# Performance work log

Measured on AMD Instinct MI355X. Metric: run time of the kernel, lower is better.

Reference implementation:

```python
import jax, jax.numpy as jnp
import numpy as np

B, C, H, W = 64, 128, 32, 32
GROUPS = 32
EPS = 1e-6
SCALE = 0.044194173824159216  # 1/sqrt(512), as hardcoded in the torch module


def setup_inputs() -> dict:
    key = jax.random.key(0)
    ks = jax.random.split(key, 12)
    s = 1.0 / np.sqrt(C)
    return {
        "x": jax.random.normal(ks[0], (B, C, H, W), dtype=jnp.float32),
        "gn_w": jax.random.normal(ks[1], (C,), dtype=jnp.float32) * 0.02 + 1.0,
        "gn_b": jax.random.normal(ks[2], (C,), dtype=jnp.float32) * 0.02,
        "wq": jax.random.uniform(ks[3], (C, C), jnp.float32, -s, s),
        "bq": jax.random.uniform(ks[4], (C,), jnp.float32, -s, s),
        "wk": jax.random.uniform(ks[5], (C, C), jnp.float32, -s, s),
        "bk": jax.random.uniform(ks[6], (C,), jnp.float32, -s, s),
        "wv": jax.random.uniform(ks[7], (C, C), jnp.float32, -s, s),
        "bv": jax.random.uniform(ks[8], (C,), jnp.float32, -s, s),
        "wo": jax.random.uniform(ks[9], (C, C), jnp.float32, -s, s),
        "bo": jax.random.uniform(ks[10], (C,), jnp.float32, -s, s),
    }


def reference(x, gn_w, gn_b, wq, bq, wk, bk, wv, bv, wo, bo):
    b = x.shape[0]
    res = x
    # GroupNorm(32 groups, 128 channels): normalize over (channels_per_group, H, W)
    xg = x.reshape(b, GROUPS, C // GROUPS, H * W)
    mean = xg.mean(axis=(2, 3), keepdims=True)
    var = xg.var(axis=(2, 3), keepdims=True)
    xn = (xg - mean) * jax.lax.rsqrt(var + EPS)
    xn = xn.reshape(b, C, H, W) * gn_w[:, None, None] + gn_b[:, None, None]
    # flatten spatial -> sequence: [b, S=1024, C=128]
    t = xn.reshape(b, C, H * W).transpose(0, 2, 1)
    q = t @ wq.T + bq
    k = t @ wk.T + bk
    v = t @ wv.T + bv
    att = jnp.einsum('bsc,btc->bst', q, k) * SCALE  # [b, S, S]
    att = jax.nn.softmax(att, axis=-1)
    o = jnp.einsum('bst,btc->bsc', att, v)
    o = o @ wo.T + bo
    out = o.transpose(0, 2, 1).reshape(b, C, H, W) + res
    return out
```

## Files before the change

kernel.cpp:

```cpp
#include <hip/hip_runtime.h>
#include <hip/hip_bf16.h>

#define BATCH 64
#define CCH 128
#define SEQ 1024
#define NG 32
#define EPSV 1e-6f
#define SCALEV 0.044194173824159216f
#define QPRE (0.044194173824159216f * 1.4426950408889634f)

typedef short v8s __attribute__((ext_vector_type(8)));
typedef short v4s __attribute__((ext_vector_type(4)));
typedef float v4f __attribute__((ext_vector_type(4)));
typedef int   v4i __attribute__((ext_vector_type(4)));
typedef unsigned short us;

__device__ __forceinline__ us f2bf(float f) {
    __hip_bfloat16 h = __float2bfloat16(f);
    return *reinterpret_cast<us*>(&h);
}

__device__ __forceinline__ int cvtpk(float lo, float hi) {
    int r;
    asm("v_cvt_pk_bf16_f32 %0, %1, %2" : "=v"(r) : "v"(lo), "v"(hi));
    return r;
}

#if __has_builtin(__builtin_amdgcn_exp2f)
#define EXP2F(x) __builtin_amdgcn_exp2f(x)
#else
#define EXP2F(x) exp2f(x)
#endif

#define MFMA16(a, b, c) __builtin_amdgcn_mfma_f32_16x16x32_bf16(a, b, c, 0, 0, 0)

__device__ __forceinline__ void gld_lds16(const us* g, us* l) {
    __builtin_amdgcn_global_load_lds(
        (const __attribute__((address_space(1))) void*)g,
        (__attribute__((address_space(3))) void*)l, 16, 0, 0);
}

__global__ void prep_gn(const float* __restrict__ wq, const float* __restrict__ wk,
                        const float* __restrict__ wv, const float* __restrict__ wo,
                        us* wbf, const float* __restrict__ x,
                        float* meanr, float* rstdr) {
    int tid = threadIdx.x;
    if (blockIdx.x < 256) {
        int i = blockIdx.x * 256 + tid;
        const float* srcs[4] = {wq, wk, wv, wo};
        wbf[i] = f2bf(srcs[i >> 14][i & 16383]);
        return;
    }
    int bg = blockIdx.x - 256;
    const float4* p = (const float4*)(x + (size_t)bg * (4 * SEQ));
    float s1 = 0.f, s2 = 0.f;
    #pragma unroll
    for (int i = 0; i < 4; i++) {
        float4 v = p[i * 256 + tid];
        s1 += v.x + v.y + v.z + v.w;
        s2 += v.x * v.x + v.y * v.y + v.z * v.z + v.w * v.w;
    }
    #pragma unroll
    for (int off = 32; off; off >>= 1) {
        s1 += __shfl_down(s1, off);
        s2 += __shfl_down(s2, off);
    }
    __shared__ float a1[4], a2[4];
    int w = tid >> 6, l = tid & 63;
    if (l == 0) { a1[w] = s1; a2[w] = s2; }
    __syncthreads();
    if (tid == 0) {
        float t1 = a1[0] + a1[1] + a1[2] + a1[3];
        float t2 = a2[0] + a2[1] + a2[2] + a2[3];
        float mean = t1 * (1.0f / (4 * SEQ));
        float var  = t2 * (1.0f / (4 * SEQ)) - mean * mean;
        meanr[bg] = mean;
        rstdr[bg] = rsqrtf(var + EPSV);
    }
}

__global__ __launch_bounds__(256, 4) void qkv_kernel(
    const float* __restrict__ x, const float* __restrict__ gn_w,
    const float* __restrict__ gn_b, const float* __restrict__ meanr,
    const float* __restrict__ rstdr, const us* __restrict__ wbf,
    const float* __restrict__ bq, const float* __restrict__ bk,
    const float* __restrict__ bv,
    us* Q, us* K, us* Vt)
{
    __shared__ us tls[9216];
    __shared__ float sa[CCH], sb[CCH];
    int b  = blockIdx.x >> 4;
    int s0 = (blockIdx.x & 15) * 64;
    int tid = threadIdx.x;
    const float* xb = x + (size_t)b * CCH * SEQ;

    if (tid < CCH) {
        int g = tid >> 2;
        float rs = rstdr[b * NG + g];
        float mu = meanr[b * NG + g];
        float a_ = rs * gn_w[tid];
        sa[tid] = a_;
        sb[tid] = gn_b[tid] - mu * a_;
    }
    __syncthreads();

    #pragma unroll
    for (int rep = 0; rep < 8; rep++) {
        int idx = rep * 256 + tid;
        int c = idx >> 4, s4 = idx & 15;
        float4 v = *(const float4*)&xb[c * SEQ + s0 + s4 * 4];
        float a_ = sa[c], b_ = sb[c];
        int sbase = s4 * 4;
        tls[(sbase + 0) * 136 + c] = f2bf(v.x * a_ + b_);
        tls[(sbase + 1) * 136 + c] = f2bf(v.y * a_ + b_);
        tls[(sbase + 2) * 136 + c] = f2bf(v.z * a_ + b_);
        tls[(sbase + 3) * 136 + c] = f2bf(v.w * a_ + b_);
    }
    __syncthreads();

    int w = tid >> 6, lane = tid & 63;
    int m = lane & 15, quad = lane >> 4;

    v8s a[4][4];
    #pragma unroll
    for (int st = 0; st < 4; st++)
        #pragma unroll
        for (int ch = 0; ch < 4; ch++)
            a[st][ch] = *(const v8s*)&tls[(st * 16 + m) * 136 + ch * 32 + quad * 8];
    __syncthreads();

    us* Qb = Q + (size_t)b * SEQ * CCH;
    us* Kb = K + (size_t)b * SEQ * CCH;
    us* Vb = Vt + (size_t)b * CCH * SEQ;

    #pragma unroll
    for (int o = 0; o < 3; o++) {
        const us* wmat = wbf + o * 16384;
        const float* bb = (o == 0) ? bq : (o == 1) ? bk : bv;
        #pragma unroll
        for (int t2 = 0; t2 < 2; t2++) {
            int T = (o * 2 + t2) * 4 + w;
            int ct = T & 7;
            int col = ct * 16 + m;
            v8s bfr[4];
            #pragma unroll
            for (int ch = 0; ch < 4; ch++)
                bfr[ch] = *(const v8s*)&wmat[(ct * 16 + m) * 128 + ch * 32 + quad * 8];
            float bias = bb[col];
            #pragma unroll
            for (int st = 0; st < 4; st++) {
                v4f acc = {0,0,0,0};
                #pragma unroll
                for (int ch = 0; ch < 4; ch++)
                    acc = MFMA16(a[st][ch], bfr[ch], acc);
                if (o < 2) {
                    #pragma unroll
                    for (int r = 0; r < 4; r++) {
                        float v = acc[r] + bias;
                        if (o == 0) v *= QPRE;
                        tls[(st * 16 + quad * 4 + r) * 136 + col] = f2bf(v);
                    }
                } else {
                    #pragma unroll
                    for (int r = 0; r < 4; r++)
                        tls[col * 72 + st * 16 + quad * 4 + r] = f2bf(acc[r] + bias);
                }
            }
        }
        __syncthreads();
        if (o < 2) {
            us* dst = (o == 0) ? Qb : Kb;
            #pragma unroll
            for (int rep = 0; rep < 4; rep++) {
                int idx = rep * 256 + tid;
                int row = idx >> 4, c8 = idx & 15;
                *(v8s*)&dst[(size_t)(s0 + row) * 128 + c8 * 8] =
                    *(const v8s*)&tls[row * 136 + c8 * 8];
            }
        } else {
            #pragma unroll
            for (int rep = 0; rep < 4; rep++) {
                int idx = rep * 256 + tid;
                int c = idx >> 3, c8 = idx & 7;
                *(v8s*)&Vb[(size_t)c * SEQ + s0 + c8 * 8] =
                    *(const v8s*)&tls[c * 72 + c8 * 8];
            }
        }
        if (o < 2) __syncthreads();
    }
}

__global__ __launch_bounds__(256, 2) void attn_kernel(
    const us* __restrict__ Q, const us* __restrict__ K,
    const us* __restrict__ Vt, const us* __restrict__ wbo,
    const float* __restrict__ bo, const float* __restrict__ x,
    float* __restrict__ out)
{
    __shared__ char smem_raw[65536];

    int i = blockIdx.x;
    int b  = (i & 7) * 8 + ((i >> 3) & 7);
    int qt = i >> 6;
    int tid = threadIdx.x;
    int w = tid >> 6, lane = tid & 63;
    int m = lane & 15, quad = lane >> 4;
    int qrow0 = qt * 128 + w * 32;
    const us* Qb = Q + (size_t)b * SEQ * CCH;
    const us* Kb = K + (size_t)b * SEQ * CCH;
    const us* Vb = Vt + (size_t)b * CCH * SEQ;

    v8s aq[2][4];
    #pragma unroll
    for (int st = 0; st < 2; st++)
        #pragma unroll
        for (int ch = 0; ch < 4; ch++)
            aq[st][ch] = *(const v8s*)&Qb[(size_t)(qrow0 + st * 16 + m) * 128 + ch * 32 + quad * 8];

    v4f oacc[2][8];
    #pragma unroll
    for (int st = 0; st < 2; st++)
        #pragma unroll
        for (int ct = 0; ct < 8; ct++) oacc[st][ct] = (v4f){0, 0, 0, 0};
    float lrun[2] = {0.f, 0.f};

    const us* kg[4]; const us* vg[4];
    int jb = w * 4;
    #pragma unroll
    for (int j4 = 0; j4 < 4; j4++) {
        int j = jb + j4;
        int kr = 4 * j + (lane >> 4);
        kg[j4] = Kb + (size_t)kr * 128 + ((lane & 15) ^ (kr & 15)) * 8;
        int vc = 8 * j + (lane >> 3);
        vg[j4] = Vb + (size_t)vc * SEQ + ((lane & 7) ^ (vc & 7)) * 8;
    }
    int idx0 = 2 * (quad & 1) * 16 + m;
    int idx1 = idx0 + 16;

    #pragma unroll
    for (int j4 = 0; j4 < 4; j4++) {
        gld_lds16(kg[j4], (us*)smem_raw + (jb + j4) * 512);
        gld_lds16(vg[j4], (us*)(smem_raw + 16384) + (jb + j4) * 512);
    }

    for (int kt = 0; kt < 16; kt++) {
        int boff  = (kt & 1) ? 32768 : 0;
        int boffn = boff ^ 32768;
        __builtin_amdgcn_s_barrier();
        if (kt < 15) {
            #pragma unroll
            for (int j4 = 0; j4 < 4; j4++) {
                gld_lds16(kg[j4] + (size_t)(kt + 1) * 8192,
                          (us*)(smem_raw + boffn) + (jb + j4) * 512);
                gld_lds16(vg[j4] + (size_t)(kt + 1) * 64,
                          (us*)(smem_raw + boffn + 16384) + (jb + j4) * 512);
            }
            asm volatile("s_waitcnt vmcnt(8)" ::: "memory");
        } else {
            asm volatile("s_waitcnt vmcnt(0)" ::: "memory");
        }
        __builtin_amdgcn_s_barrier();

        const us* kl = (const us*)(smem_raw + boff);
        const us* vl = (const us*)(smem_raw + boff + 16384);

        __builtin_amdgcn_s_setprio(1);

        v4f acc0[4], acc1[4];
        int e[2][4][2];

        #define QK_STEP(c2) { \
            int krow = (c2) * 16 + m; \
            v4f A0 = {0,0,0,0}, A1 = {0,0,0,0}; \
            _Pragma("unroll") \
            for (int ch = 0; ch < 4; ch++) { \
                int chunk = (ch * 4 + quad) ^ (krow & 15); \
                v8s kb = *(const v8s*)&kl[krow * 128 + chunk * 8]; \
                A0 = MFMA16(kb, aq[0][ch], A0); \
                A1 = MFMA16(kb, aq[1][ch], A1); \
            } \
            acc0[c2] = A0; acc1[c2] = A1; }

        #define EXP_STEP(c2) { \
            float p0[4], p1[4]; \
            _Pragma("unroll") \
            for (int r = 0; r < 4; r++) { \
                p0[r] = EXP2F(acc0[c2][r]); \
                p1[r] = EXP2F(acc1[c2][r]); \
                lrun[0] += p0[r]; lrun[1] += p1[r]; \
            } \
            e[0][c2][0] = cvtpk(p0[0], p0[1]); e[0][c2][1] = cvtpk(p0[2], p0[3]); \
            e[1][c2][0] = cvtpk(p1[0], p1[1]); e[1][c2][1] = cvtpk(p1[2], p1[3]); }

        QK_STEP(0)
        QK_STEP(1)
        EXP_STEP(0)
        QK_STEP(2)
        EXP_STEP(1)
        QK_STEP(3)
        EXP_STEP(2)
        EXP_STEP(3)

        #define SHFL_STEP(kc2, paw) { \
            _Pragma("unroll") \
            for (int st = 0; st < 2; st++) { \
                int c0 = (quad < 2) ? e[st][2 * (kc2)][0] : e[st][2 * (kc2) + 1][0]; \
                int c1 = (quad < 2) ? e[st][2 * (kc2)][1] : e[st][2 * (kc2) + 1][1]; \
                v4i t; \
                t[0] = __shfl(c0, idx0); \
                t[1] = __shfl(c1, idx0); \
                t[2] = __shfl(c0, idx1); \
                t[3] = __shfl(c1, idx1); \
                paw[st] = __builtin_bit_cast(v8s, t); } }

        v8s pa0[2], pa1[2];
        SHFL_STEP(0, pa0)
        #pragma unroll
        for (int ct = 0; ct < 8; ct++) {
            int vrow = ct * 16 + m;
            int chunk = quad ^ (vrow & 7);
            v8s vb = *(const v8s*)&vl[vrow * 64 + chunk * 8];
            oacc[0][ct] = MFMA16(pa0[0], vb, oacc[0][ct]);
            oacc[1][ct] = MFMA16(pa0[1], vb, oacc[1][ct]);
        }
        SHFL_STEP(1, pa1)
        #pragma unroll
        for (int ct = 0; ct < 8; ct++) {
            int vrow = ct * 16 + m;
            int chunk = (4 + quad) ^ (vrow & 7);
            v8s vb = *(const v8s*)&vl[vrow * 64 + chunk * 8];
            oacc[0][ct] = MFMA16(pa1[0], vb, oacc[0][ct]);
            oacc[1][ct] = MFMA16(pa1[1], vb, oacc[1][ct]);
        }
        __builtin_amdgcn_s_setprio(0);
        #undef QK_STEP
        #undef EXP_STEP
        #undef SHFL_STEP
    }

    float inv[2][4];
    #pragma unroll
    for (int st = 0; st < 2; st++) {
        float rs = lrun[st];
        rs += __shfl_xor(rs, 16);
        rs += __shfl_xor(rs, 32);
        #pragma unroll
        for (int r = 0; r < 4; r++)
            inv[st][r] = 1.0f / __shfl(rs, quad * 4 + r);
    }
    __syncthreads();
    us* olds = (us*)smem_raw;
    #pragma unroll
    for (int st = 0; st < 2; st++)
        #pragma unroll
        for (int ct = 0; ct < 8; ct++)
            #pragma unroll
            for (int r = 0; r < 4; r++)
                olds[(w * 32 + st * 16 + quad * 4 + r) * 136 + ct * 16 + m] =
                    f2bf(oacc[st][ct][r] * inv[st][r]);
    __syncthreads();

    const float* xb = x + (size_t)b * CCH * SEQ;
    float* ob = out + (size_t)b * CCH * SEQ;
    int sbase = qt * 128 + w * 32;
    v8s obf[2][4];
    #pragma unroll
    for (int st = 0; st < 2; st++)
        #pragma unroll
        for (int ch = 0; ch < 4; ch++)
            obf[st][ch] = *(const v8s*)&olds[(w * 32 + st * 16 + m) * 136 + ch * 32 + quad * 8];
    #pragma unroll
    for (int mt = 0; mt < 8; mt++) {
        v8s af[4];
        #pragma unroll
        for (int ch = 0; ch < 4; ch++)
            af[ch] = *(const v8s*)&wbo[(mt * 16 + m) * 128 + ch * 32 + quad * 8];
        #pragma unroll
        for (int st = 0; st < 2; st++) {
            v4f acc = {0,0,0,0};
            #pragma unroll
            for (int ch = 0; ch < 4; ch++)
                acc = MFMA16(af[ch], obf[st][ch], acc);
            #pragma unroll
            for (int r = 0; r < 4; r++) {
                int c = mt * 16 + quad * 4 + r;
                int idx = c * SEQ + sbase + st * 16 + m;
                ob[idx] = acc[r] + bo[c] + xb[idx];
            }
        }
    }
}

extern "C" void kernel_launch(void* const* d_in, const int* in_sizes, int n_in,
                              void* d_out, int out_size, void* d_ws, size_t ws_size,
                              hipStream_t stream) {
    const float* x    = (const float*)d_in[0];
    const float* gn_w = (const float*)d_in[1];
    const float* gn_b = (const float*)d_in[2];
    const float* wq   = (const float*)d_in[3];
    const float* bq   = (const float*)d_in[4];
    const float* wk   = (const float*)d_in[5];
    const float* bk   = (const float*)d_in[6];
    const float* wv   = (const float*)d_in[7];
    const float* bv   = (const float*)d_in[8];
    const float* wo   = (const float*)d_in[9];
    const float* bo   = (const float*)d_in[10];
    float* out = (float*)d_out;

    char* ws = (char*)d_ws;
    us* wbf      = (us*)ws;
    float* meanr = (float*)(ws + 131072);
    float* rstdr = (float*)(ws + 139264);
    us* Qbuf     = (us*)(ws + 147456);
    us* Kbuf     = (us*)(ws + 147456 + 16777216ull);
    us* Vtbuf    = (us*)(ws + 147456 + 2ull * 16777216ull);

    prep_gn<<<256 + BATCH * NG, 256, 0, stream>>>(wq, wk, wv, wo, wbf, x, meanr, rstdr);
    qkv_kernel<<<1024, 256, 0, stream>>>(x, gn_w, gn_b, meanr, rstdr, wbf,
                                         bq, bk, bv, Qbuf, Kbuf, Vtbuf);
    attn_kernel<<<512, 256, 0, stream>>>(Qbuf, Kbuf, Vtbuf, wbf + 3 * 16384,
                                         bo, x, out);
}
```

Baseline: 166.5 us.

## Split KV tile across warp pairs with 64 query rows per warp

Each warp now owns 64 query rows and processes half of each 64-key tile, instead of 32 query rows over the full tile. Every K and V fragment read from LDS therefore feeds four MFMAs instead of two, cutting LDS traffic per MFMA. The two key-halves are combined at the end through an LDS reduction of the row sums and fp32 output accumulators. The cost is doubled accumulator registers (oacc grows to 128 floats), which may pressure the two-blocks-per-CU occupancy target, plus extra epilogue barriers.

Result: slower. 180.6 us (+8.5%).

```diff
diff --git a/kernel.cpp b/kernel.cpp
--- a/kernel.cpp
+++ b/kernel.cpp
@@ -203,25 +203,26 @@
     int qt = i >> 6;
     int tid = threadIdx.x;
     int w = tid >> 6, lane = tid & 63;
+    int qs = w & 1, kh = w >> 1;
     int m = lane & 15, quad = lane >> 4;
-    int qrow0 = qt * 128 + w * 32;
+    int qrow0 = qt * 128 + qs * 64;
     const us* Qb = Q + (size_t)b * SEQ * CCH;
     const us* Kb = K + (size_t)b * SEQ * CCH;
     const us* Vb = Vt + (size_t)b * CCH * SEQ;
 
-    v8s aq[2][4];
-    #pragma unroll
-    for (int st = 0; st < 2; st++)
+    v8s aq[4][4];
+    #pragma unroll
+    for (int st = 0; st < 4; st++)
         #pragma unroll
         for (int ch = 0; ch < 4; ch++)
             aq[st][ch] = *(const v8s*)&Qb[(size_t)(qrow0 + st * 16 + m) * 128 + ch * 32 + quad * 8];
 
-    v4f oacc[2][8];
-    #pragma unroll
-    for (int st = 0; st < 2; st++)
+    v4f oacc[4][8];
+    #pragma unroll
+    for (int st = 0; st < 4; st++)
         #pragma unroll
         for (int ct = 0; ct < 8; ct++) oacc[st][ct] = (v4f){0, 0, 0, 0};
-    float lrun[2] = {0.f, 0.f};
+    float lrun[4] = {0.f, 0.f, 0.f, 0.f};
 
     const us* kg[4]; const us* vg[4];
     int jb = w * 4;
@@ -265,98 +266,124 @@
 
         __builtin_amdgcn_s_setprio(1);
 
-        v4f acc0[4], acc1[4];
-        int e[2][4][2];
-
-        #define QK_STEP(c2) { \
-            int krow = (c2) * 16 + m; \
-            v4f A0 = {0,0,0,0}, A1 = {0,0,0,0}; \
-            _Pragma("unroll") \
-            for (int ch = 0; ch < 4; ch++) { \
-                int chunk = (ch * 4 + quad) ^ (krow & 15); \
-                v8s kb = *(const v8s*)&kl[krow * 128 + chunk * 8]; \
-                A0 = MFMA16(kb, aq[0][ch], A0); \
-                A1 = MFMA16(kb, aq[1][ch], A1); \
-            } \
-            acc0[c2] = A0; acc1[c2] = A1; }
-
-        #define EXP_STEP(c2) { \
-            float p0[4], p1[4]; \
-            _Pragma("unroll") \
-            for (int r = 0; r < 4; r++) { \
-                p0[r] = EXP2F(acc0[c2][r]); \
-                p1[r] = EXP2F(acc1[c2][r]); \
-                lrun[0] += p0[r]; lrun[1] += p1[r]; \
-            } \
-            e[0][c2][0] = cvtpk(p0[0], p0[1]); e[0][c2][1] = cvtpk(p0[2], p0[3]); \
-            e[1][c2][0] = cvtpk(p1[0], p1[1]); e[1][c2][1] = cvtpk(p1[2], p1[3]); }
-
-        QK_STEP(0)
-        QK_STEP(1)
-        EXP_STEP(0)
-        QK_STEP(2)
-        EXP_STEP(1)
-        QK_STEP(3)
-        EXP_STEP(2)
-        EXP_STEP(3)
-
-        #define SHFL_STEP(kc2, paw) { \
-            _Pragma("unroll") \
-            for (int st = 0; st < 2; st++) { \
-                int c0 = (quad < 2) ? e[st][2 * (kc2)][0] : e[st][2 * (kc2) + 1][0]; \
-                int c1 = (quad < 2) ? e[st][2 * (kc2)][1] : e[st][2 * (kc2) + 1][1]; \
-                v4i t; \
-                t[0] = __shfl(c0, idx0); \
-                t[1] = __shfl(c1, idx0); \
-                t[2] = __shfl(c0, idx1); \
-                t[3] = __shfl(c1, idx1); \
-                paw[st] = __builtin_bit_cast(v8s, t); } }
-
-        v8s pa0[2], pa1[2];
-        SHFL_STEP(0, pa0)
+        int e[4][2][2];
+
+        #pragma unroll
+        for (int c2 = 0; c2 < 2; c2++) {
+            int krow = kh * 32 + c2 * 16 + m;
+            v4f A0 = {0,0,0,0}, A1 = {0,0,0,0}, A2 = {0,0,0,0}, A3 = {0,0,0,0};
+            #pragma unroll
+            for (int ch = 0; ch < 4; ch++) {
+                int chunk = (ch * 4 + quad) ^ m;
+                v8s kb = *(const v8s*)&kl[krow * 128 + chunk * 8];
+                A0 = MFMA16(kb, aq[0][ch], A0);
+                A1 = MFMA16(kb, aq[1][ch], A1);
+                A2 = MFMA16(kb, aq[2][ch], A2);
+                A3 = MFMA16(kb, aq[3][ch], A3);
+            }
+            float p[4][4];
+            #pragma unroll
+            for (int r = 0; r < 4; r++) {
+                p[0][r] = EXP2F(A0[r]);
+                p[1][r] = EXP2F(A1[r]);
+                p[2][r] = EXP2F(A2[r]);
+                p[3][r] = EXP2F(A3[r]);
+            }
+            #pragma unroll
+            for (int st = 0; st < 4; st++) {
+                lrun[st] += p[st][0] + p[st][1] + p[st][2] + p[st][3];
+                e[st][c2][0] = cvtpk(p[st][0], p[st][1]);
+                e[st][c2][1] = cvtpk(p[st][2], p[st][3]);
+            }
+        }
+
+        v8s pa[4];
+        #pragma unroll
+        for (int st = 0; st < 4; st++) {
+            int c0 = (quad < 2) ? e[st][0][0] : e[st][1][0];
+            int c1 = (quad < 2) ? e[st][0][1] : e[st][1][1];
+            v4i t;
+            t[0] = __shfl(c0, idx0);
+            t[1] = __shfl(c1, idx0);
+            t[2] = __shfl(c0, idx1);
+            t[3] = __shfl(c1, idx1);
+            pa[st] = __builtin_bit_cast(v8s, t);
+        }
         #pragma unroll
         for (int ct = 0; ct < 8; ct++) {
             int vrow = ct * 16 + m;
-            int chunk = quad ^ (vrow & 7);
+            int chunk = (kh * 4 + quad) ^ (vrow & 7);
             v8s vb = *(const v8s*)&vl[vrow * 64 + chunk * 8];
-            oacc[0][ct] = MFMA16(pa0[0], vb, oacc[0][ct]);
-            oacc[1][ct] = MFMA16(pa0[1], vb, oacc[1][ct]);
-        }
-        SHFL_STEP(1, pa1)
-        #pragma unroll
-        for (int ct = 0; ct < 8; ct++) {
-            int vrow = ct * 16 + m;
-            int chunk = (4 + quad) ^ (vrow & 7);
-            v8s vb = *(const v8s*)&vl[vrow * 64 + chunk * 8];
-            oacc[0][ct] = MFMA16(pa1[0], vb, oacc[0][ct]);
-            oacc[1][ct] = MFMA16(pa1[1], vb, oacc[1][ct]);
+            oacc[0][ct] = MFMA16(pa[0], vb, oacc[0][ct]);
+            oacc[1][ct] = MFMA16(pa[1], vb, oacc[1][ct]);
+            oacc[2][ct] = MFMA16(pa[2], vb, oacc[2][ct]);
+            oacc[3][ct] = MFMA16(pa[3], vb, oacc[3][ct]);
         }
         __builtin_amdgcn_s_setprio(0);
-        #undef QK_STEP
-        #undef EXP_STEP
-        #undef SHFL_STEP
-    }
-
-    float inv[2][4];
-    #pragma unroll
-    for (int st = 0; st < 2; st++) {
-        float rs = lrun[st];
-        rs += __shfl_xor(rs, 16);
-        rs += __shfl_xor(rs, 32);
-        #pragma unroll
-        for (int r = 0; r < 4; r++)
-            inv[st][r] = 1.0f / __shfl(rs, quad * 4 + r);
+    }
+
+    float rs[4];
+    #pragma unroll
+    for (int st = 0; st < 4; st++) {
+        float r_ = lrun[st];
+        r_ += __shfl_xor(r_, 16);
+        r_ += __shfl_xor(r_, 32);
+        rs[st] = r_;
+    }
+    __syncthreads();
+    float* lf = (float*)smem_raw;
+    if (quad == 0) {
+        #pragma unroll
+        for (int st = 0; st < 4; st++)
+            lf[kh * 128 + qs * 64 + st * 16 + m] = rs[st];
+    }
+    __syncthreads();
+    float inv_[4][4];
+    #pragma unroll
+    for (int st = 0; st < 4; st++) {
+        v4f la = *(const v4f*)&lf[qs * 64 + st * 16 + quad * 4];
+        v4f lb = *(const v4f*)&lf[128 + qs * 64 + st * 16 + quad * 4];
+        #pragma unroll
+        for (int r = 0; r < 4; r++) inv_[st][r] = 1.0f / (la[r] + lb[r]);
+    }
+    __syncthreads();
+    float* Oa = (float*)smem_raw;
+    if (kh == 0) {
+        #pragma unroll
+        for (int st = 0; st < 4; st++)
+            #pragma unroll
+            for (int ct = 0; ct < 8; ct++)
+                #pragma unroll
+                for (int r = 0; r < 4; r++)
+                    Oa[(qs * 64 + st * 16 + quad * 4 + r) * 128 +
+                       ((ct * 16 + m) ^ ((quad & 1) << 4))] = oacc[st][ct][r];
+    }
+    __syncthreads();
+    if (kh == 1) {
+        #pragma unroll
+        for (int st = 0; st < 4; st++)
+            #pragma unroll
+            for (int ct = 0; ct < 8; ct++)
+                #pragma unroll
+                for (int r = 0; r < 4; r++) {
+                    float v = oacc[st][ct][r] +
+                        Oa[(qs * 64 + st * 16 + quad * 4 + r) * 128 +
+                           ((ct * 16 + m) ^ ((quad & 1) << 4))];
+                    oacc[st][ct][r] = v * inv_[st][r];
+                }
     }
     __syncthreads();
     us* olds = (us*)smem_raw;
-    #pragma unroll
-    for (int st = 0; st < 2; st++)
-        #pragma unroll
-        for (int ct = 0; ct < 8; ct++)
-            #pragma unroll
-            for (int r = 0; r < 4; r++)
-                olds[(w * 32 + st * 16 + quad * 4 + r) * 136 + ct * 16 + m] =
-                    f2bf(oacc[st][ct][r] * inv[st][r]);
+    if (kh == 1) {
+        #pragma unroll
+        for (int st = 0; st < 4; st++)
+            #pragma unroll
+            for (int ct = 0; ct < 8; ct++)
+                #pragma unroll
+                for (int r = 0; r < 4; r++)
+                    olds[(qs * 64 + st * 16 + quad * 4 + r) * 136 + ct * 16 + m] =
+                        f2bf(oacc[st][ct][r]);
+    }
     __syncthreads();
 
     const float* xb = x + (size_t)b * CCH * SEQ;
```

## Software-pipeline attention loop so PV of previous tile overlaps QK/exp

Applied to the files above, without the earlier changes.

Restructures the attention main loop into a skewed pipeline: each iteration computes QK^T and exp for the current key tile while doing the P·V MFMAs for the previous tile, with an extra epilogue iteration. V now uses a triple-buffered LDS ring (LDS grows from 64KB to 80KB) so the previous tile's V stays live while the next one loads. The aim is to interleave exp/VALU work with matrix ops and hide the dependency chain. The larger LDS footprint may lower occupancy below the 2 blocks per CU requested by the launch bounds, and carrying the probabilities across iterations raises register pressure.

After: 165.0 us. About the same (-0.9%).

```diff
diff --git a/kernel.cpp b/kernel.cpp
--- a/kernel.cpp
+++ b/kernel.cpp
@@ -196,7 +196,7 @@
     const float* __restrict__ bo, const float* __restrict__ x,
     float* __restrict__ out)
 {
-    __shared__ char smem_raw[65536];
+    __shared__ char smem_raw[81920];
 
     int i = blockIdx.x;
     int b  = (i & 7) * 8 + ((i >> 3) & 7);
@@ -239,29 +239,33 @@
     #pragma unroll
     for (int j4 = 0; j4 < 4; j4++) {
         gld_lds16(kg[j4], (us*)smem_raw + (jb + j4) * 512);
-        gld_lds16(vg[j4], (us*)(smem_raw + 16384) + (jb + j4) * 512);
-    }
-
-    for (int kt = 0; kt < 16; kt++) {
-        int boff  = (kt & 1) ? 32768 : 0;
-        int boffn = boff ^ 32768;
-        __builtin_amdgcn_s_barrier();
-        if (kt < 15) {
-            #pragma unroll
-            for (int j4 = 0; j4 < 4; j4++) {
-                gld_lds16(kg[j4] + (size_t)(kt + 1) * 8192,
-                          (us*)(smem_raw + boffn) + (jb + j4) * 512);
-                gld_lds16(vg[j4] + (size_t)(kt + 1) * 64,
-                          (us*)(smem_raw + boffn + 16384) + (jb + j4) * 512);
-            }
-            asm volatile("s_waitcnt vmcnt(8)" ::: "memory");
-        } else {
-            asm volatile("s_waitcnt vmcnt(0)" ::: "memory");
-        }
-        __builtin_amdgcn_s_barrier();
-
-        const us* kl = (const us*)(smem_raw + boff);
-        const us* vl = (const us*)(smem_raw + boff + 16384);
+        gld_lds16(vg[j4], (us*)(smem_raw + 32768) + (jb + j4) * 512);
+    }
+
+    v8s cpa0[2], cpa1[2];
+
+    for (int kt = 0; kt <= 16; kt++) {
+        if (kt < 16) {
+            __builtin_amdgcn_s_barrier();
+            if (kt < 15) {
+                int kb_n = ((kt + 1) & 1) * 16384;
+                int vb_n = 32768 + ((kt + 1) % 3) * 16384;
+                #pragma unroll
+                for (int j4 = 0; j4 < 4; j4++) {
+                    gld_lds16(kg[j4] + (size_t)(kt + 1) * 8192,
+                              (us*)(smem_raw + kb_n) + (jb + j4) * 512);
+                    gld_lds16(vg[j4] + (size_t)(kt + 1) * 64,
+                              (us*)(smem_raw + vb_n) + (jb + j4) * 512);
+                }
+                asm volatile("s_waitcnt vmcnt(8)" ::: "memory");
+            } else {
+                asm volatile("s_waitcnt vmcnt(0)" ::: "memory");
+            }
+            __builtin_amdgcn_s_barrier();
+        }
+
+        const us* kl = (const us*)(smem_raw + (kt & 1) * 16384);
+        const us* vp = (const us*)(smem_raw + 32768 + ((kt + 2) % 3) * 16384);
 
         __builtin_amdgcn_s_setprio(1);
 
@@ -291,50 +295,53 @@
             e[0][c2][0] = cvtpk(p0[0], p0[1]); e[0][c2][1] = cvtpk(p0[2], p0[3]); \
             e[1][c2][0] = cvtpk(p1[0], p1[1]); e[1][c2][1] = cvtpk(p1[2], p1[3]); }
 
-        QK_STEP(0)
-        QK_STEP(1)
-        EXP_STEP(0)
-        QK_STEP(2)
-        EXP_STEP(1)
-        QK_STEP(3)
-        EXP_STEP(2)
-        EXP_STEP(3)
-
-        #define SHFL_STEP(kc2, paw) { \
+        #define PV_HALF(kc2, paw) { \
             _Pragma("unroll") \
-            for (int st = 0; st < 2; st++) { \
-                int c0 = (quad < 2) ? e[st][2 * (kc2)][0] : e[st][2 * (kc2) + 1][0]; \
-                int c1 = (quad < 2) ? e[st][2 * (kc2)][1] : e[st][2 * (kc2) + 1][1]; \
-                v4i t; \
-                t[0] = __shfl(c0, idx0); \
-                t[1] = __shfl(c1, idx0); \
-                t[2] = __shfl(c0, idx1); \
-                t[3] = __shfl(c1, idx1); \
-                paw[st] = __builtin_bit_cast(v8s, t); } }
-
-        v8s pa0[2], pa1[2];
-        SHFL_STEP(0, pa0)
-        #pragma unroll
-        for (int ct = 0; ct < 8; ct++) {
-            int vrow = ct * 16 + m;
-            int chunk = quad ^ (vrow & 7);
-            v8s vb = *(const v8s*)&vl[vrow * 64 + chunk * 8];
-            oacc[0][ct] = MFMA16(pa0[0], vb, oacc[0][ct]);
-            oacc[1][ct] = MFMA16(pa0[1], vb, oacc[1][ct]);
-        }
-        SHFL_STEP(1, pa1)
-        #pragma unroll
-        for (int ct = 0; ct < 8; ct++) {
-            int vrow = ct * 16 + m;
-            int chunk = (4 + quad) ^ (vrow & 7);
-            v8s vb = *(const v8s*)&vl[vrow * 64 + chunk * 8];
-            oacc[0][ct] = MFMA16(pa1[0], vb, oacc[0][ct]);
-            oacc[1][ct] = MFMA16(pa1[1], vb, oacc[1][ct]);
+            for (int ct = 0; ct < 8; ct++) { \
+                int vrow = ct * 16 + m; \
+                int chunk = ((kc2) * 4 + quad) ^ (vrow & 7); \
+                v8s vb = *(const v8s*)&vp[vrow * 64 + chunk * 8]; \
+                oacc[0][ct] = MFMA16(paw[0], vb, oacc[0][ct]); \
+                oacc[1][ct] = MFMA16(paw[1], vb, oacc[1][ct]); } }
+
+        if (kt < 16) {
+            QK_STEP(0)
+            QK_STEP(1)
+            QK_STEP(2)
+            QK_STEP(3)
+        }
+        if (kt > 0) PV_HALF(0, cpa0)
+        if (kt < 16) {
+            EXP_STEP(0)
+            EXP_STEP(1)
+        }
+        if (kt > 0) PV_HALF(1, cpa1)
+        if (kt < 16) {
+            EXP_STEP(2)
+            EXP_STEP(3)
+            #pragma unroll
+            for (int st = 0; st < 2; st++) {
+                int c0 = (quad < 2) ? e[st][0][0] : e[st][1][0];
+                int c1 = (quad < 2) ? e[st][0][1] : e[st][1][1];
+                v4i t;
+                t[0] = __shfl(c0, idx0);
+                t[1] = __shfl(c1, idx0);
+                t[2] = __shfl(c0, idx1);
+                t[3] = __shfl(c1, idx1);
+                cpa0[st] = __builtin_bit_cast(v8s, t);
+                c0 = (quad < 2) ? e[st][2][0] : e[st][3][0];
+                c1 = (quad < 2) ? e[st][2][1] : e[st][3][1];
+                t[0] = __shfl(c0, idx0);
+                t[1] = __shfl(c1, idx0);
+                t[2] = __shfl(c0, idx1);
+                t[3] = __shfl(c1, idx1);
+                cpa1[st] = __builtin_bit_cast(v8s, t);
+            }
         }
         __builtin_amdgcn_s_setprio(0);
         #undef QK_STEP
         #undef EXP_STEP
-        #undef SHFL_STEP
+        #undef PV_HALF
     }
 
     float inv[2][4];
```
